# Performance work log

Hardware: AMD Instinct MI355X
Metric: run time of the kernel (lower is better)

Reference implementation:

```python
import jax, jax.numpy as jnp
import numpy as np

H_PATCH = 32
W_PATCH = 32
DIM = 512
HEADS = 8
DIM_HEAD = 64
INNER = HEADS * DIM_HEAD
N = H_PATCH * W_PATCH
BATCH = 32


def make_relative_position_index(h, w):
    coords = np.stack(np.meshgrid(np.arange(h), np.arange(w), indexing='ij'))  # [2,h,w]
    flat = coords.reshape(2, -1)  # [2, N]
    rel = flat[:, :, None] - flat[:, None, :]  # [2, N, N]
    rel = rel.transpose(1, 2, 0).copy()  # [N, N, 2]
    rel[:, :, 0] += h - 1
    rel[:, :, 1] += w - 1
    rel[:, :, 0] *= 2 * h - 1
    return jnp.asarray(rel.sum(-1), dtype=jnp.int32)  # [N, N]


def setup_inputs() -> dict:
    key = jax.random.key(0)
    k1, k2, k3, k4 = jax.random.split(key, 4)
    x = jax.random.normal(k1, (BATCH, N, DIM), dtype=jnp.float32)
    w_qkv = jax.random.normal(k2, (DIM, 3 * INNER), dtype=jnp.float32) * (DIM ** -0.5)
    w_out = jax.random.normal(k3, (INNER, DIM), dtype=jnp.float32) * (INNER ** -0.5)
    b_out = jnp.zeros((DIM,), dtype=jnp.float32)
    bias_table = jax.random.normal(k4, ((2 * H_PATCH - 1) * (2 * W_PATCH - 1), HEADS), dtype=jnp.float32) * 0.02
    rel_index = make_relative_position_index(H_PATCH, W_PATCH)
    return {"x": x, "w_qkv": w_qkv, "w_out": w_out, "b_out": b_out,
            "bias_table": bias_table, "rel_index": rel_index}


def reference(x, w_qkv, w_out, b_out, bias_table, rel_index):
    b, n, _ = x.shape
    scale = DIM_HEAD ** -0.5
    qkv = x @ w_qkv  # [b, n, 3*inner]
    q, k, v = jnp.split(qkv, 3, axis=-1)
    def heads(t):
        return t.reshape(b, n, HEADS, DIM_HEAD).transpose(0, 2, 1, 3)  # [b,h,n,d]
    q, k, v = heads(q), heads(k), heads(v)
    dots = jnp.einsum('bhnd,bhmd->bhnm', q, k) * scale  # [b,h,n,n]
    bias = bias_table[rel_index]  # [n,n,heads]
    dots = dots + bias.transpose(2, 0, 1)[None]  # [b,h,n,n]
    attn = jax.nn.softmax(dots, axis=-1)
    out = jnp.einsum('bhnm,bhmd->bhnd', attn, v)
    out = out.transpose(0, 2, 1, 3).reshape(b, n, INNER)
    return out @ w_out + b_out
```

## Files before the change

### kernel.cpp

```cpp
#include <hip/hip_runtime.h>
#include <stdint.h>

typedef unsigned short u16;
typedef __attribute__((ext_vector_type(8))) short short8;
typedef __attribute__((ext_vector_type(4))) float floatx4;

__device__ __forceinline__ u16 f2bf(float f) {
  union { float f; unsigned u; } v; v.f = f;
  return (u16)((v.u + 0x7FFFu + ((v.u >> 16) & 1u)) >> 16);
}
__device__ __forceinline__ void gl_lds16(const void* g, void* l) {
  __builtin_amdgcn_global_load_lds((const __attribute__((address_space(1))) void*)g,
                                   (__attribute__((address_space(3))) void*)l, 16, 0, 0);
}
__device__ __forceinline__ float exp2_fast(float x) {
#if __has_builtin(__builtin_amdgcn_exp2f)
  return __builtin_amdgcn_exp2f(x);
#else
  return exp2f(x);
#endif
}

__global__ __launch_bounds__(256) void k_cast_x(const float* __restrict__ x, u16* __restrict__ xb) {
  int t = blockIdx.x * 256 + threadIdx.x;
  const float4* xv = (const float4*)x;
  float4 a = xv[2 * t], b = xv[2 * t + 1];
  short8 o;
  o[0] = f2bf(a.x); o[1] = f2bf(a.y); o[2] = f2bf(a.z); o[3] = f2bf(a.w);
  o[4] = f2bf(b.x); o[5] = f2bf(b.y); o[6] = f2bf(b.z); o[7] = f2bf(b.w);
  ((short8*)xb)[t] = o;
}

__global__ __launch_bounds__(256) void k_prep_w(const float* __restrict__ wqkv, const float* __restrict__ wout,
                                                u16* __restrict__ wqkvT, u16* __restrict__ woutT) {
  int t = blockIdx.x * 256 + threadIdx.x;
  if (t < 786432) {
    int n = t >> 9, k = t & 511;
    wqkvT[t] = f2bf(wqkv[k * 1536 + n]);
  } else {
    int u = t - 786432;
    int n = u >> 9, k = u & 511;
    woutT[u] = f2bf(wout[k * 512 + n]);
  }
}

__global__ __launch_bounds__(256) void k_prep_bias(const int* __restrict__ rel, const float* __restrict__ tab,
                                                   u16* __restrict__ biasb) {
  int t = blockIdx.x * 256 + threadIdx.x;
  int r    = t & 3;
  int ti   = (t >> 2) & 1;
  int l15  = (t >> 3) & 15;
  int quad = (t >> 7) & 3;
  int w    = (t >> 9) & 3;
  int kt   = (t >> 11) & 7;
  int qt   = (t >> 14) & 7;
  int h    = t >> 17;
  int qrow = qt * 128 + w * 32 + ti * 16 + quad * 4 + r;
  const int* rr = rel + qrow * 1024 + kt * 128 + l15;
  short8 o;
  #pragma unroll
  for (int tj = 0; tj < 8; tj++) {
    int idx = rr[tj * 16];
    o[tj] = f2bf((tab[idx * 8 + h] - 8.0f) * 1.44269504f);
  }
  ((short8*)biasb)[t] = o;
}

__global__ __launch_bounds__(256) void k_gemm_qkv(const u16* __restrict__ xb, const u16* __restrict__ wT,
                                                  u16* __restrict__ qbuf, u16* __restrict__ kbuf,
                                                  u16* __restrict__ vtbuf) {
  __shared__ u16 sm[17408];
  const int bn = blockIdx.x, bm = blockIdx.y;
  const int tid = threadIdx.x, w = tid >> 6, lane = tid & 63;
  const int quad = lane >> 4, l15 = lane & 15;
  const int wr = w >> 1, wc = w & 1;
  const u16* Ag = xb + (size_t)bm * 128 * 512;
  const u16* Bg = wT + (size_t)bn * 128 * 512;
  floatx4 acc[4][4];
  floatx4 zero = {0.f, 0.f, 0.f, 0.f};
  #pragma unroll
  for (int i = 0; i < 4; i++)
    #pragma unroll
    for (int j = 0; j < 4; j++) acc[i][j] = zero;

  for (int kb = 0; kb < 512; kb += 32) {
    __syncthreads();
    #pragma unroll
    for (int i = 0; i < 2; i++) {
      int c = w * 128 + i * 64 + lane;
      int row = c >> 2, col = (c & 3) * 8;
      gl_lds16(Ag + (size_t)row * 512 + kb + col, &sm[(w * 128 + i * 64) * 8]);
      gl_lds16(Bg + (size_t)row * 512 + kb + col, &sm[4096 + (w * 128 + i * 64) * 8]);
    }
    __syncthreads();
    short8 af[4], bf[4];
    #pragma unroll
    for (int ti = 0; ti < 4; ti++)
      af[ti] = *(const short8*)&sm[(wr * 64 + ti * 16 + l15) * 32 + quad * 8];
    #pragma unroll
    for (int tj = 0; tj < 4; tj++)
      bf[tj] = *(const short8*)&sm[4096 + (wc * 64 + tj * 16 + l15) * 32 + quad * 8];
    #pragma unroll
    for (int ti = 0; ti < 4; ti++)
      #pragma unroll
      for (int tj = 0; tj < 4; tj++)
        acc[ti][tj] = __builtin_amdgcn_mfma_f32_16x16x32_bf16(af[ti], bf[tj], acc[ti][tj], 0, 0, 0);
  }
  __syncthreads();
  #pragma unroll
  for (int ti = 0; ti < 4; ti++)
    #pragma unroll
    for (int tj = 0; tj < 4; tj++)
      #pragma unroll
      for (int r = 0; r < 4; r++)
        sm[(wr * 64 + ti * 16 + quad * 4 + r) * 136 + wc * 64 + tj * 16 + l15] = f2bf(acc[ti][tj][r]);
  __syncthreads();
  const int b = bm >> 3;
  const int nrow0 = (bm & 7) * 128;
  if (bn < 8) {
    u16* dst = (bn < 4) ? qbuf : kbuf;
    #pragma unroll
    for (int i = 0; i < 8; i++) {
      int chunk = i * 256 + tid;
      int r = chunk >> 4, c8 = chunk & 15;
      int nin = (bn & 3) * 128 + c8 * 8;
      int h = nin >> 6, d = nin & 63;
      uint4 val = *(const uint4*)&sm[r * 136 + c8 * 8];
      *(uint4*)&dst[(((size_t)(b * 8 + h)) * 1024 + nrow0 + r) * 64 + d] = val;
    }
  } else {
    #pragma unroll
    for (int i = 0; i < 8; i++) {
      int chunk = i * 256 + tid;
      int dcol = chunk & 127, nr8 = chunk >> 7;
      int nin = (bn & 3) * 128 + dcol;
      int h = nin >> 6, d = nin & 63;
      short8 v;
      #pragma unroll
      for (int j = 0; j < 8; j++) v[j] = (short)sm[(nr8 * 8 + j) * 136 + dcol];
      *(short8*)&vtbuf[(((size_t)(b * 8 + h)) * 64 + d) * 1024 + nrow0 + nr8 * 8] = v;
    }
  }
}

__global__ __launch_bounds__(256, 2) void k_attn(const u16* __restrict__ qbuf, const u16* __restrict__ kbuf,
                                                 const u16* __restrict__ vtbuf, const u16* __restrict__ biasb,
                                                 u16* __restrict__ attn_out) {
  __shared__ u16 sm[40960];
  const int PO = 32768;
  const int b = blockIdx.x, h = blockIdx.y >> 3, qt = blockIdx.y & 7;
  const int tid = threadIdx.x, w = tid >> 6, lane = tid & 63;
  const int quad = lane >> 4, l15 = lane & 15;
  const int xm = l15 & 7;
  u16* pw = &sm[PO + w * 2048];
  const size_t bh = (size_t)(b * 8 + h);
  const u16* qg = qbuf + (bh * 1024 + (size_t)qt * 128) * 64;
  const u16* kg = kbuf + bh * 1024 * 64;
  const u16* vg = vtbuf + bh * 64 * 1024;
  const u16* bg = biasb + (size_t)h * 1048576 + (size_t)qt * 131072 +
                  (size_t)w * 4096 + quad * 1024 + l15 * 64;

  int rK[4], cK[4], dV[4], cV[4];
  #pragma unroll
  for (int i = 0; i < 4; i++) {
    int p = (w * 4 + i) * 64 + lane;
    rK[i] = p >> 3;  cK[i] = (p & 7) ^ (rK[i] & 7);
    dV[i] = p >> 4;  cV[i] = (p & 15) ^ (dV[i] & 7);
  }

  short8 qf[2][2];
  #pragma unroll
  for (int ti = 0; ti < 2; ti++)
    #pragma unroll
    for (int kk = 0; kk < 2; kk++)
      qf[ti][kk] = *(const short8*)&qg[(w * 32 + ti * 16 + l15) * 64 + kk * 32 + quad * 8];

  floatx4 oacc[2][4];
  floatx4 zero = {0.f, 0.f, 0.f, 0.f};
  #pragma unroll
  for (int i = 0; i < 2; i++)
    #pragma unroll
    for (int j = 0; j < 4; j++) oacc[i][j] = zero;
  float lrow[2][4];
  #pragma unroll
  for (int i = 0; i < 2; i++)
    #pragma unroll
    for (int r = 0; r < 4; r++) lrow[i][r] = 0.f;

  const float SC = 0.125f * 1.44269504f;

  #pragma unroll
  for (int i = 0; i < 4; i++) {
    gl_lds16(kg + (size_t)rK[i] * 64 + cK[i] * 8, &sm[(w * 4 + i) * 512]);
    gl_lds16(vg + (size_t)dV[i] * 1024 + cV[i] * 8, &sm[8192 + (w * 4 + i) * 512]);
  }
  __syncthreads();

  for (int kt = 0; kt < 8; kt++) {
    const int cur = (kt & 1) ? 16384 : 0;
    const int nxt = (kt & 1) ? 0 : 16384;
    if (kt < 7) {
      #pragma unroll
      for (int i = 0; i < 4; i++) {
        gl_lds16(kg + (size_t)((kt + 1) * 128 + rK[i]) * 64 + cK[i] * 8, &sm[nxt + (w * 4 + i) * 512]);
        gl_lds16(vg + (size_t)dV[i] * 1024 + (kt + 1) * 128 + cV[i] * 8, &sm[nxt + 8192 + (w * 4 + i) * 512]);
      }
    }
    const u16* bkt = bg + kt * 16384;
    uint2 bu[2][4][2];
    #pragma unroll
    for (int ti = 0; ti < 2; ti++)
      #pragma unroll
      for (int r = 0; r < 4; r++) {
        bu[ti][r][0] = *(const uint2*)&bkt[(ti * 4 + r) * 8];
        bu[ti][r][1] = *(const uint2*)&bkt[(ti * 4 + r) * 8 + 4];
      }

    #pragma unroll
    for (int tjh = 0; tjh < 2; tjh++) {
      floatx4 sacc[2][4];
      #pragma unroll
      for (int tjl = 0; tjl < 4; tjl++) { sacc[0][tjl] = zero; sacc[1][tjl] = zero; }
      #pragma unroll
      for (int tjl = 0; tjl < 4; tjl++) {
        int tj = tjh * 4 + tjl;
        #pragma unroll
        for (int kk = 0; kk < 2; kk++) {
          short8 kf = *(const short8*)&sm[cur + (tj * 16 + l15) * 64 + ((kk * 4 + quad) ^ xm) * 8];
          sacc[0][tjl] = __builtin_amdgcn_mfma_f32_16x16x32_bf16(qf[0][kk], kf, sacc[0][tjl], 0, 0, 0);
          sacc[1][tjl] = __builtin_amdgcn_mfma_f32_16x16x32_bf16(qf[1][kk], kf, sacc[1][tjl], 0, 0, 0);
        }
      }
      #pragma unroll
      for (int ti = 0; ti < 2; ti++)
        #pragma unroll
        for (int r = 0; r < 4; r++) {
          int lr = ti * 16 + quad * 4 + r;
          int wm = lr & 7;
          unsigned blo = bu[ti][r][tjh].x, bhi = bu[ti][r][tjh].y;
          float bf32[4];
          bf32[0] = __builtin_bit_cast(float, blo << 16);
          bf32[1] = __builtin_bit_cast(float, blo & 0xFFFF0000u);
          bf32[2] = __builtin_bit_cast(float, bhi << 16);
          bf32[3] = __builtin_bit_cast(float, bhi & 0xFFFF0000u);
          float rs = 0.f;
          #pragma unroll
          for (int tjl = 0; tjl < 4; tjl++) {
            float p = exp2_fast(sacc[ti][tjl][r] * SC + bf32[tjl]);
            rs += p;
            unsigned pu = __builtin_bit_cast(unsigned, p);
            int cc = (tjl * 2 + (l15 >> 3)) ^ wm;
            pw[lr * 64 + cc * 8 + xm] = (u16)((pu + 0x8000u) >> 16);
          }
          lrow[ti][r] += rs;
        }
      #pragma unroll
      for (int kbl = 0; kbl < 2; kbl++) {
        short8 pf0 = *(const short8*)&pw[l15 * 64 + ((kbl * 4 + quad) ^ xm) * 8];
        short8 pf1 = *(const short8*)&pw[(16 + l15) * 64 + ((kbl * 4 + quad) ^ xm) * 8];
        #pragma unroll
        for (int dj = 0; dj < 4; dj++) {
          int kc = (tjh * 8 + kbl * 4 + quad) ^ xm;
          short8 vf = *(const short8*)&sm[cur + 8192 + (dj * 16 + l15) * 128 + kc * 8];
          oacc[0][dj] = __builtin_amdgcn_mfma_f32_16x16x32_bf16(pf0, vf, oacc[0][dj], 0, 0, 0);
          oacc[1][dj] = __builtin_amdgcn_mfma_f32_16x16x32_bf16(pf1, vf, oacc[1][dj], 0, 0, 0);
        }
      }
    }
    __syncthreads();
  }

  #pragma unroll
  for (int ti = 0; ti < 2; ti++)
    #pragma unroll
    for (int r = 0; r < 4; r++) {
      float s = lrow[ti][r];
      s += __shfl_xor(s, 1); s += __shfl_xor(s, 2);
      s += __shfl_xor(s, 4); s += __shfl_xor(s, 8);
      float inv = 1.f / s;
      int row = w * 32 + ti * 16 + quad * 4 + r;
      size_t ob = ((size_t)(b * 1024 + qt * 128 + row)) * 512 + h * 64;
      #pragma unroll
      for (int dj = 0; dj < 4; dj++)
        attn_out[ob + dj * 16 + l15] = f2bf(oacc[ti][dj][r] * inv);
    }
}

__global__ __launch_bounds__(256) void k_gemm_out(const u16* __restrict__ ab, const u16* __restrict__ wT,
                                                  const float* __restrict__ bout, float* __restrict__ out) {
  __shared__ u16 sm[8192];
  const int bn = blockIdx.x, bm = blockIdx.y;
  const int tid = threadIdx.x, w = tid >> 6, lane = tid & 63;
  const int quad = lane >> 4, l15 = lane & 15;
  const int wr = w >> 1, wc = w & 1;
  const u16* Ag = ab + (size_t)bm * 128 * 512;
  const u16* Bg = wT + (size_t)bn * 128 * 512;
  float bv[4];
  #pragma unroll
  for (int tj = 0; tj < 4; tj++) bv[tj] = bout[bn * 128 + wc * 64 + tj * 16 + l15];
  floatx4 acc[4][4];
  floatx4 zero = {0.f, 0.f, 0.f, 0.f};
  #pragma unroll
  for (int i = 0; i < 4; i++)
    #pragma unroll
    for (int j = 0; j < 4; j++) acc[i][j] = zero;

  for (int kb = 0; kb < 512; kb += 32) {
    __syncthreads();
    #pragma unroll
    for (int i = 0; i < 2; i++) {
      int c = w * 128 + i * 64 + lane;
      int row = c >> 2, col = (c & 3) * 8;
      gl_lds16(Ag + (size_t)row * 512 + kb + col, &sm[(w * 128 + i * 64) * 8]);
      gl_lds16(Bg + (size_t)row * 512 + kb + col, &sm[4096 + (w * 128 + i * 64) * 8]);
    }
    __syncthreads();
    short8 af[4], bf[4];
    #pragma unroll
    for (int ti = 0; ti < 4; ti++)
      af[ti] = *(const short8*)&sm[(wr * 64 + ti * 16 + l15) * 32 + quad * 8];
    #pragma unroll
    for (int tj = 0; tj < 4; tj++)
      bf[tj] = *(const short8*)&sm[4096 + (wc * 64 + tj * 16 + l15) * 32 + quad * 8];
    #pragma unroll
    for (int ti = 0; ti < 4; ti++)
      #pragma unroll
      for (int tj = 0; tj < 4; tj++)
        acc[ti][tj] = __builtin_amdgcn_mfma_f32_16x16x32_bf16(af[ti], bf[tj], acc[ti][tj], 0, 0, 0);
  }
  #pragma unroll
  for (int ti = 0; ti < 4; ti++)
    #pragma unroll
    for (int tj = 0; tj < 4; tj++)
      #pragma unroll
      for (int r = 0; r < 4; r++) {
        int row = bm * 128 + wr * 64 + ti * 16 + quad * 4 + r;
        int colg = bn * 128 + wc * 64 + tj * 16 + l15;
        out[(size_t)row * 512 + colg] = acc[ti][tj][r] + bv[tj];
      }
}

extern "C" void kernel_launch(void* const* d_in, const int* in_sizes, int n_in,
                              void* d_out, int out_size, void* d_ws, size_t ws_size,
                              hipStream_t stream) {
  const float* x    = (const float*)d_in[0];
  const float* wqkv = (const float*)d_in[1];
  const float* wout = (const float*)d_in[2];
  const float* bout = (const float*)d_in[3];
  const float* btab = (const float*)d_in[4];
  const int*   rel  = (const int*)d_in[5];
  char* ws = (char*)d_ws;
  u16* xb    = (u16*)(ws + 0);
  u16* qbuf  = (u16*)(ws + 33554432);
  u16* kbuf  = (u16*)(ws + 67108864);
  u16* vtbuf = (u16*)(ws + 100663296);
  u16* biasb = (u16*)(ws + 134217728);
  u16* wqkvT = (u16*)(ws + 150994944);
  u16* woutT = (u16*)(ws + 152567808);
  float* out = (float*)d_out;

  k_cast_x  <<<8192, 256, 0, stream>>>(x, xb);
  k_prep_w  <<<4096, 256, 0, stream>>>(wqkv, wout, wqkvT, woutT);
  k_prep_bias<<<4096, 256, 0, stream>>>(rel, btab, biasb);
  k_gemm_qkv<<<dim3(12, 256), 256, 0, stream>>>(xb, wqkvT, qbuf, kbuf, vtbuf);
  k_attn    <<<dim3(32, 64), 256, 0, stream>>>(qbuf, kbuf, vtbuf, biasb, xb);
  k_gemm_out<<<dim3(4, 256), 256, 0, stream>>>(xb, woutT, bout, out);
}
```

Measured before the change: 388.3 us.

## Compute transposed scores so P stays in registers, removing LDS round-trip

Result: slower. 398.4 us (+2.6%).

```diff
diff --git a/kernel.cpp b/kernel.cpp
--- a/kernel.cpp
+++ b/kernel.cpp
@@ -3,7 +3,16 @@
 
 typedef unsigned short u16;
 typedef __attribute__((ext_vector_type(8))) short short8;
+typedef __attribute__((ext_vector_type(4))) short bf16x4;
 typedef __attribute__((ext_vector_type(4))) float floatx4;
+typedef __attribute__((ext_vector_type(2))) int int2v;
+
+#define MFMA32(a, b, c) __builtin_amdgcn_mfma_f32_16x16x32_bf16(a, b, c, 0, 0, 0)
+#if __has_builtin(__builtin_amdgcn_mfma_f32_16x16x16bf16_1k)
+#define MFMA16(a, b, c) __builtin_amdgcn_mfma_f32_16x16x16bf16_1k(a, b, c, 0, 0, 0)
+#else
+#define MFMA16(a, b, c) (c)
+#endif
 
 __device__ __forceinline__ u16 f2bf(float f) {
   union { float f; unsigned u; } v; v.f = f;
@@ -19,6 +28,11 @@
 #else
   return exp2f(x);
 #endif
+}
+__device__ __forceinline__ unsigned pk2bf(float a, float b) {
+  unsigned ua = __builtin_bit_cast(unsigned, a);
+  unsigned ub = __builtin_bit_cast(unsigned, b);
+  return ((ua + 0x8000u) >> 16) | ((ub + 0x8000u) & 0xFFFF0000u);
 }
 
 __global__ __launch_bounds__(256) void k_cast_x(const float* __restrict__ x, u16* __restrict__ xb) {
@@ -47,23 +61,23 @@
 __global__ __launch_bounds__(256) void k_prep_bias(const int* __restrict__ rel, const float* __restrict__ tab,
                                                    u16* __restrict__ biasb) {
   int t = blockIdx.x * 256 + threadIdx.x;
-  int r    = t & 3;
-  int ti   = (t >> 2) & 1;
-  int l15  = (t >> 3) & 15;
-  int quad = (t >> 7) & 3;
-  int w    = (t >> 9) & 3;
-  int kt   = (t >> 11) & 7;
-  int qt   = (t >> 14) & 7;
-  int h    = t >> 17;
-  int qrow = qt * 128 + w * 32 + ti * 16 + quad * 4 + r;
-  const int* rr = rel + qrow * 1024 + kt * 128 + l15;
-  short8 o;
-  #pragma unroll
-  for (int tj = 0; tj < 8; tj++) {
-    int idx = rr[tj * 16];
-    o[tj] = f2bf((tab[idx * 8 + h] - 8.0f) * 1.44269504f);
-  }
-  ((short8*)biasb)[t] = o;
+  int lane = t & 63;
+  int qi   = (t >> 6) & 1;
+  int kvt  = (t >> 7) & 7;
+  int w    = (t >> 10) & 3;
+  int kt   = (t >> 12) & 7;
+  int qt   = (t >> 15) & 7;
+  int h    = t >> 18;
+  int q  = qt * 128 + w * 32 + qi * 16 + (lane & 15);
+  int kv = kt * 128 + kvt * 16 + (lane >> 4) * 4;
+  const int* rr = rel + q * 1024 + kv;
+  bf16x4 o;
+  #pragma unroll
+  for (int r = 0; r < 4; r++) {
+    int idx = rr[r];
+    o[r] = (short)f2bf((tab[idx * 8 + h] - 8.0f) * 1.44269504f);
+  }
+  ((bf16x4*)biasb)[t] = o;
 }
 
 __global__ __launch_bounds__(256) void k_gemm_qkv(const u16* __restrict__ xb, const u16* __restrict__ wT,
@@ -104,7 +118,7 @@
     for (int ti = 0; ti < 4; ti++)
       #pragma unroll
       for (int tj = 0; tj < 4; tj++)
-        acc[ti][tj] = __builtin_amdgcn_mfma_f32_16x16x32_bf16(af[ti], bf[tj], acc[ti][tj], 0, 0, 0);
+        acc[ti][tj] = MFMA32(af[ti], bf[tj], acc[ti][tj]);
   }
   __syncthreads();
   #pragma unroll
@@ -138,7 +152,12 @@
       short8 v;
       #pragma unroll
       for (int j = 0; j < 8; j++) v[j] = (short)sm[(nr8 * 8 + j) * 136 + dcol];
-      *(short8*)&vtbuf[(((size_t)(b * 8 + h)) * 64 + d) * 1024 + nrow0 + nr8 * 8] = v;
+      int n0 = nr8 * 8;
+      int kb = n0 >> 5, u = (n0 >> 4) & 1, qd0 = (n0 >> 2) & 3;
+      int pos0 = kb * 32 + qd0 * 8 + u * 4;
+      u16* dst = &vtbuf[(((size_t)(b * 8 + h)) * 64 + d) * 1024 + nrow0 + pos0];
+      *(bf16x4*)&dst[0] = __builtin_shufflevector(v, v, 0, 1, 2, 3);
+      *(bf16x4*)&dst[8] = __builtin_shufflevector(v, v, 4, 5, 6, 7);
     }
   }
 }
@@ -146,19 +165,16 @@
 __global__ __launch_bounds__(256, 2) void k_attn(const u16* __restrict__ qbuf, const u16* __restrict__ kbuf,
                                                  const u16* __restrict__ vtbuf, const u16* __restrict__ biasb,
                                                  u16* __restrict__ attn_out) {
-  __shared__ u16 sm[40960];
-  const int PO = 32768;
+  __shared__ u16 sm[32768];
   const int b = blockIdx.x, h = blockIdx.y >> 3, qt = blockIdx.y & 7;
   const int tid = threadIdx.x, w = tid >> 6, lane = tid & 63;
   const int quad = lane >> 4, l15 = lane & 15;
   const int xm = l15 & 7;
-  u16* pw = &sm[PO + w * 2048];
   const size_t bh = (size_t)(b * 8 + h);
   const u16* qg = qbuf + (bh * 1024 + (size_t)qt * 128) * 64;
   const u16* kg = kbuf + bh * 1024 * 64;
   const u16* vg = vtbuf + bh * 64 * 1024;
-  const u16* bg = biasb + (size_t)h * 1048576 + (size_t)qt * 131072 +
-                  (size_t)w * 4096 + quad * 1024 + l15 * 64;
+  const u16* bg = biasb + (size_t)h * 1048576 + (size_t)qt * 131072 + (size_t)w * 4096 + lane * 4;
 
   int rK[4], cK[4], dV[4], cV[4];
   #pragma unroll
@@ -170,22 +186,18 @@
 
   short8 qf[2][2];
   #pragma unroll
-  for (int ti = 0; ti < 2; ti++)
+  for (int qi = 0; qi < 2; qi++)
     #pragma unroll
     for (int kk = 0; kk < 2; kk++)
-      qf[ti][kk] = *(const short8*)&qg[(w * 32 + ti * 16 + l15) * 64 + kk * 32 + quad * 8];
-
-  floatx4 oacc[2][4];
+      qf[qi][kk] = *(const short8*)&qg[(w * 32 + qi * 16 + l15) * 64 + kk * 32 + quad * 8];
+
+  floatx4 oacc[4][2];
   floatx4 zero = {0.f, 0.f, 0.f, 0.f};
   #pragma unroll
-  for (int i = 0; i < 2; i++)
-    #pragma unroll
-    for (int j = 0; j < 4; j++) oacc[i][j] = zero;
-  float lrow[2][4];
-  #pragma unroll
-  for (int i = 0; i < 2; i++)
-    #pragma unroll
-    for (int r = 0; r < 4; r++) lrow[i][r] = 0.f;
+  for (int dj = 0; dj < 4; dj++)
+    #pragma unroll
+    for (int qi = 0; qi < 2; qi++) oacc[dj][qi] = zero;
+  float lrow[2] = {0.f, 0.f};
 
   const float SC = 0.125f * 1.44269504f;
 
@@ -207,63 +219,59 @@
       }
     }
     const u16* bkt = bg + kt * 16384;
-    uint2 bu[2][4][2];
-    #pragma unroll
-    for (int ti = 0; ti < 2; ti++)
-      #pragma unroll
-      for (int r = 0; r < 4; r++) {
-        bu[ti][r][0] = *(const uint2*)&bkt[(ti * 4 + r) * 8];
-        bu[ti][r][1] = *(const uint2*)&bkt[(ti * 4 + r) * 8 + 4];
-      }
 
     #pragma unroll
     for (int tjh = 0; tjh < 2; tjh++) {
-      floatx4 sacc[2][4];
-      #pragma unroll
-      for (int tjl = 0; tjl < 4; tjl++) { sacc[0][tjl] = zero; sacc[1][tjl] = zero; }
-      #pragma unroll
-      for (int tjl = 0; tjl < 4; tjl++) {
-        int tj = tjh * 4 + tjl;
+      uint2 bu[4][2];
+      #pragma unroll
+      for (int kl = 0; kl < 4; kl++)
+        #pragma unroll
+        for (int qi = 0; qi < 2; qi++)
+          bu[kl][qi] = *(const uint2*)&bkt[((tjh * 4 + kl) * 2 + qi) * 256];
+      floatx4 sacc[4][2];
+      #pragma unroll
+      for (int kl = 0; kl < 4; kl++) { sacc[kl][0] = zero; sacc[kl][1] = zero; }
+      #pragma unroll
+      for (int kl = 0; kl < 4; kl++) {
+        int kvt = tjh * 4 + kl;
         #pragma unroll
         for (int kk = 0; kk < 2; kk++) {
-          short8 kf = *(const short8*)&sm[cur + (tj * 16 + l15) * 64 + ((kk * 4 + quad) ^ xm) * 8];
-          sacc[0][tjl] = __builtin_amdgcn_mfma_f32_16x16x32_bf16(qf[0][kk], kf, sacc[0][tjl], 0, 0, 0);
-          sacc[1][tjl] = __builtin_amdgcn_mfma_f32_16x16x32_bf16(qf[1][kk], kf, sacc[1][tjl], 0, 0, 0);
+          short8 kf = *(const short8*)&sm[cur + (kvt * 16 + l15) * 64 + ((kk * 4 + quad) ^ xm) * 8];
+          sacc[kl][0] = MFMA32(kf, qf[0][kk], sacc[kl][0]);
+          sacc[kl][1] = MFMA32(kf, qf[1][kk], sacc[kl][1]);
         }
       }
-      #pragma unroll
-      for (int ti = 0; ti < 2; ti++)
+      bf16x4 pk[4][2];
+      #pragma unroll
+      for (int kl = 0; kl < 4; kl++)
         #pragma unroll
-        for (int r = 0; r < 4; r++) {
-          int lr = ti * 16 + quad * 4 + r;
-          int wm = lr & 7;
-          unsigned blo = bu[ti][r][tjh].x, bhi = bu[ti][r][tjh].y;
-          float bf32[4];
-          bf32[0] = __builtin_bit_cast(float, blo << 16);
-          bf32[1] = __builtin_bit_cast(float, blo & 0xFFFF0000u);
-          bf32[2] = __builtin_bit_cast(float, bhi << 16);
-          bf32[3] = __builtin_bit_cast(float, bhi & 0xFFFF0000u);
-          float rs = 0.f;
-          #pragma unroll
-          for (int tjl = 0; tjl < 4; tjl++) {
-            float p = exp2_fast(sacc[ti][tjl][r] * SC + bf32[tjl]);
-            rs += p;
-            unsigned pu = __builtin_bit_cast(unsigned, p);
-            int cc = (tjl * 2 + (l15 >> 3)) ^ wm;
-            pw[lr * 64 + cc * 8 + xm] = (u16)((pu + 0x8000u) >> 16);
-          }
-          lrow[ti][r] += rs;
+        for (int qi = 0; qi < 2; qi++) {
+          unsigned blo = bu[kl][qi].x, bhi = bu[kl][qi].y;
+          float b0 = __builtin_bit_cast(float, blo << 16);
+          float b1 = __builtin_bit_cast(float, blo & 0xFFFF0000u);
+          float b2 = __builtin_bit_cast(float, bhi << 16);
+          float b3 = __builtin_bit_cast(float, bhi & 0xFFFF0000u);
+          float p0 = exp2_fast(sacc[kl][qi][0] * SC + b0);
+          float p1 = exp2_fast(sacc[kl][qi][1] * SC + b1);
+          float p2 = exp2_fast(sacc[kl][qi][2] * SC + b2);
+          float p3 = exp2_fast(sacc[kl][qi][3] * SC + b3);
+          lrow[qi] += (p0 + p1) + (p2 + p3);
+          int2v pp = {(int)pk2bf(p0, p1), (int)pk2bf(p2, p3)};
+          pk[kl][qi] = __builtin_bit_cast(bf16x4, pp);
         }
       #pragma unroll
       for (int kbl = 0; kbl < 2; kbl++) {
-        short8 pf0 = *(const short8*)&pw[l15 * 64 + ((kbl * 4 + quad) ^ xm) * 8];
-        short8 pf1 = *(const short8*)&pw[(16 + l15) * 64 + ((kbl * 4 + quad) ^ xm) * 8];
+        int kb = tjh * 2 + kbl;
         #pragma unroll
         for (int dj = 0; dj < 4; dj++) {
-          int kc = (tjh * 8 + kbl * 4 + quad) ^ xm;
-          short8 vf = *(const short8*)&sm[cur + 8192 + (dj * 16 + l15) * 128 + kc * 8];
-          oacc[0][dj] = __builtin_amdgcn_mfma_f32_16x16x32_bf16(pf0, vf, oacc[0][dj], 0, 0, 0);
-          oacc[1][dj] = __builtin_amdgcn_mfma_f32_16x16x32_bf16(pf1, vf, oacc[1][dj], 0, 0, 0);
+          short8 vv = *(const short8*)&sm[cur + 8192 + (dj * 16 + l15) * 128 + ((kb * 4 + quad) ^ xm) * 8];
+          bf16x4 vlo = __builtin_shufflevector(vv, vv, 0, 1, 2, 3);
+          bf16x4 vhi = __builtin_shufflevector(vv, vv, 4, 5, 6, 7);
+          #pragma unroll
+          for (int qi = 0; qi < 2; qi++) {
+            oacc[dj][qi] = MFMA16(vlo, pk[kbl * 2 + 0][qi], oacc[dj][qi]);
+            oacc[dj][qi] = MFMA16(vhi, pk[kbl * 2 + 1][qi], oacc[dj][qi]);
+          }
         }
       }
     }
@@ -271,19 +279,20 @@
   }
 
   #pragma unroll
-  for (int ti = 0; ti < 2; ti++)
-    #pragma unroll
-    for (int r = 0; r < 4; r++) {
-      float s = lrow[ti][r];
-      s += __shfl_xor(s, 1); s += __shfl_xor(s, 2);
-      s += __shfl_xor(s, 4); s += __shfl_xor(s, 8);
-      float inv = 1.f / s;
-      int row = w * 32 + ti * 16 + quad * 4 + r;
-      size_t ob = ((size_t)(b * 1024 + qt * 128 + row)) * 512 + h * 64;
-      #pragma unroll
-      for (int dj = 0; dj < 4; dj++)
-        attn_out[ob + dj * 16 + l15] = f2bf(oacc[ti][dj][r] * inv);
-    }
+  for (int qi = 0; qi < 2; qi++) {
+    float s = lrow[qi];
+    s += __shfl_xor(s, 16);
+    s += __shfl_xor(s, 32);
+    float inv = 1.f / s;
+    int n = b * 1024 + qt * 128 + w * 32 + qi * 16 + l15;
+    #pragma unroll
+    for (int dj = 0; dj < 4; dj++) {
+      unsigned lo = ((unsigned)f2bf(oacc[dj][qi][0] * inv)) | ((unsigned)f2bf(oacc[dj][qi][1] * inv) << 16);
+      unsigned hi = ((unsigned)f2bf(oacc[dj][qi][2] * inv)) | ((unsigned)f2bf(oacc[dj][qi][3] * inv) << 16);
+      int2v o = {(int)lo, (int)hi};
+      *(int2v*)&attn_out[(size_t)n * 512 + h * 64 + dj * 16 + quad * 4] = o;
+    }
+  }
 }
 
 __global__ __launch_bounds__(256) void k_gemm_out(const u16* __restrict__ ab, const u16* __restrict__ wT,
@@ -326,7 +335,7 @@
     for (int ti = 0; ti < 4; ti++)
       #pragma unroll
       for (int tj = 0; tj < 4; tj++)
-        acc[ti][tj] = __builtin_amdgcn_mfma_f32_16x16x32_bf16(af[ti], bf[tj], acc[ti][tj], 0, 0, 0);
+        acc[ti][tj] = MFMA32(af[ti], bf[tj], acc[ti][tj]);
   }
   #pragma unroll
   for (int ti = 0; ti < 4; ti++)
@@ -361,7 +370,7 @@
 
   k_cast_x  <<<8192, 256, 0, stream>>>(x, xb);
   k_prep_w  <<<4096, 256, 0, stream>>>(wqkv, wout, wqkvT, woutT);
-  k_prep_bias<<<4096, 256, 0, stream>>>(rel, btab, biasb);
+  k_prep_bias<<<8192, 256, 0, stream>>>(rel, btab, biasb);
   k_gemm_qkv<<<dim3(12, 256), 256, 0, stream>>>(xb, wqkvT, qbuf, kbuf, vtbuf);
   k_attn    <<<dim3(32, 64), 256, 0, stream>>>(qbuf, kbuf, vtbuf, biasb, xb);
   k_gemm_out<<<dim3(4, 256), 256, 0, stream>>>(xb, woutT, bout, out);
```
